# Kernel optimization log

Measured on AMD Instinct MI355X. Metric: run time of the kernel, lower is better.

## Reference

```python
import jax, jax.numpy as jnp
import numpy as np

B, S, D, H = 4, 2048, 1024, 16
HD = D // H


def setup_inputs() -> dict:
    key = jax.random.key(0)
    ks = jax.random.split(key, 9)
    s = 1.0 / np.sqrt(D)
    return {
        "x": jax.random.normal(ks[0], (B, S, D), dtype=jnp.float32),
        "Wq": jax.random.uniform(ks[1], (D, D), jnp.float32, -s, s),
        "bq": jax.random.uniform(ks[2], (D,), jnp.float32, -s, s),
        "Wk": jax.random.uniform(ks[3], (D, D), jnp.float32, -s, s),
        "bk": jax.random.uniform(ks[4], (D,), jnp.float32, -s, s),
        "Wv": jax.random.uniform(ks[5], (D, D), jnp.float32, -s, s),
        "bv": jax.random.uniform(ks[6], (D,), jnp.float32, -s, s),
        "Wo": jax.random.uniform(ks[7], (D, D), jnp.float32, -s, s),
        "bo": jax.random.uniform(ks[8], (D,), jnp.float32, -s, s),
    }


def reference(x, Wq, bq, Wk, bk, Wv, bv, Wo, bo):
    b, s, _ = x.shape
    # projections (torch Linear: y = x @ W.T + b; here W stored as [D,D], use x@W for equivalent math)
    q = (x @ Wq + bq).reshape(b, s, H, HD).transpose(0, 2, 1, 3)  # [b,h,s,hd]
    k = (x @ Wk + bk).reshape(b, s, H, HD).transpose(0, 2, 1, 3)
    v = (x @ Wv + bv).reshape(b, s, H, HD).transpose(0, 2, 1, 3)
    scale = 1.0 / np.sqrt(HD).astype(np.float32)
    scores = jnp.einsum("bhqd,bhkd->bhqk", q, k) * scale  # [b,h,s,s]
    attn = jax.nn.softmax(scores, axis=-1)
    out = jnp.einsum("bhqk,bhkd->bhqd", attn, v)  # [b,h,s,hd]
    out = out.transpose(0, 2, 1, 3).reshape(b, s, D)
    return out @ Wo + bo
```

## Files before the change

### kernel.cpp

```cpp
#include <hip/hip_runtime.h>
#include <hip/hip_bf16.h>

#define NB 4
#define NS 2048
#define ND 1024
#define NH 16
#define NHD 64
#define NM (NB * NS)

typedef __attribute__((ext_vector_type(8))) short bf16x8;
typedef __attribute__((ext_vector_type(4))) float f32x4;
typedef __attribute__((ext_vector_type(16))) float f32x16;
typedef __attribute__((ext_vector_type(4))) unsigned int u32x4;

typedef const unsigned int __attribute__((address_space(1)))* gas_t;
typedef unsigned int __attribute__((address_space(3)))* las_t;

__device__ __forceinline__ void gload_lds16(const void* g, void* l) {
  __builtin_amdgcn_global_load_lds((gas_t)g, (las_t)l, 16, 0, 0);
}

__device__ __forceinline__ unsigned short f2bf(float f) {
  union { __hip_bfloat16 h; unsigned short u; } cv;
  cv.h = __float2bfloat16(f);
  return cv.u;
}

__device__ __forceinline__ unsigned int cvtpk(float a, float b) {
  unsigned int r;
  asm("v_cvt_pk_bf16_f32 %0, %1, %2" : "=v"(r) : "v"(a), "v"(b));
  return r;
}

__device__ __forceinline__ float fexp2(float x) {
  return __builtin_amdgcn_exp2f(x);
}

__global__ __launch_bounds__(256) void convert_x(
    const float* __restrict__ in, uint4* __restrict__ out) {
  const int c = blockIdx.x * 256 + threadIdx.x;
  const float4 a = *(const float4*)(in + (size_t)c * 8);
  const float4 b = *(const float4*)(in + (size_t)c * 8 + 4);
  uint4 u;
  u.x = cvtpk(a.x, a.y); u.y = cvtpk(a.z, a.w);
  u.z = cvtpk(b.x, b.y); u.w = cvtpk(b.z, b.w);
  out[c] = u;
}

__global__ __launch_bounds__(256) void transpose_qkv(
    const float* __restrict__ Wq, const float* __restrict__ Wk,
    const float* __restrict__ Wv, unsigned short* __restrict__ out) {
  __shared__ float tile[64][65];
  const int t = threadIdx.x;
  const int bx = blockIdx.x;
  const int by = blockIdx.y;
  const int which = by >> 4;
  const float* in = which == 0 ? Wq : (which == 1 ? Wk : Wv);
  const int byl = by & 15;
#pragma unroll
  for (int j = 0; j < 4; ++j) {
    const int lin = j * 1024 + t * 4;
    const int r = lin >> 6, c = lin & 63;
    float4 v = *(const float4*)(in + (size_t)(bx * 64 + r) * ND + byl * 64 + c);
    tile[r][c + 0] = v.x; tile[r][c + 1] = v.y;
    tile[r][c + 2] = v.z; tile[r][c + 3] = v.w;
  }
  __syncthreads();
#pragma unroll
  for (int j = 0; j < 4; ++j) {
    const int lin = j * 1024 + t * 4;
    const int r = lin >> 6, c = lin & 63;
    uint2 u;
    u.x = cvtpk(tile[c + 0][r], tile[c + 1][r]);
    u.y = cvtpk(tile[c + 2][r], tile[c + 3][r]);
    *(uint2*)(out + (size_t)(by * 64 + r) * ND + bx * 64 + c) = u;
  }
}

__global__ __launch_bounds__(256) void transpose_w(
    const float* __restrict__ in, unsigned short* __restrict__ out) {
  __shared__ float tile[64][65];
  const int t = threadIdx.x;
  const int bx = blockIdx.x, by = blockIdx.y;
#pragma unroll
  for (int j = 0; j < 4; ++j) {
    const int lin = j * 1024 + t * 4;
    const int r = lin >> 6, c = lin & 63;
    float4 v = *(const float4*)(in + (size_t)(bx * 64 + r) * ND + by * 64 + c);
    tile[r][c + 0] = v.x; tile[r][c + 1] = v.y;
    tile[r][c + 2] = v.z; tile[r][c + 3] = v.w;
  }
  __syncthreads();
#pragma unroll
  for (int j = 0; j < 4; ++j) {
    const int lin = j * 1024 + t * 4;
    const int r = lin >> 6, c = lin & 63;
    uint2 u;
    u.x = cvtpk(tile[c + 0][r], tile[c + 1][r]);
    u.y = cvtpk(tile[c + 2][r], tile[c + 3][r]);
    *(uint2*)(out + (size_t)(by * 64 + r) * ND + bx * 64 + c) = u;
  }
}

__global__ __launch_bounds__(256) void gemm_qkv(
    const unsigned short* __restrict__ Ab, const unsigned short* __restrict__ BT,
    const float* __restrict__ bq, const float* __restrict__ bk,
    const float* __restrict__ bv, unsigned short* __restrict__ Qb,
    unsigned short* __restrict__ Kb, unsigned short* __restrict__ VTb) {
  __shared__ unsigned short As[128 * 64];
  __shared__ unsigned short Bs[128 * 64];
  const int t = threadIdx.x;
  const int w = blockIdx.x;
  const int xcd = w & 7, idx = w >> 3;
  const int mblk = xcd + ((idx / 24) << 3);
  const int nblk = idx % 24;
  const int m0 = mblk * 128, n0 = nblk * 128;
  const int lane = t & 63, wid = t >> 6;
  const int wm = (wid >> 1) * 64, wn = (wid & 1) * 64;
  const int lr = lane & 15, lg = lane >> 4;

  const f32x4 zero4 = {0.f, 0.f, 0.f, 0.f};
  f32x4 acc[4][4];
#pragma unroll
  for (int i = 0; i < 4; ++i)
#pragma unroll
    for (int j = 0; j < 4; ++j) acc[i][j] = zero4;

  for (int k0 = 0; k0 < ND; k0 += 64) {
    __syncthreads();
#pragma unroll
    for (int j = 0; j < 4; ++j) {
      const int id = j * 256 + t;
      const int row = id >> 3, cs8 = id & 7;
      const int cg8 = cs8 ^ (row & 7);
      gload_lds16(BT + (size_t)(n0 + row) * ND + k0 + cg8 * 8, &Bs[id * 8]);
      gload_lds16(Ab + (size_t)(m0 + row) * ND + k0 + cg8 * 8, &As[id * 8]);
    }
    __syncthreads();

#pragma unroll
    for (int kk = 0; kk < 2; ++kk) {
      bf16x8 af[4], bv4[4];
#pragma unroll
      for (int mi = 0; mi < 4; ++mi) {
        const int row = wm + mi * 16 + lr;
        const int slot = (kk * 4 + lg) ^ (row & 7);
        af[mi] = *(const bf16x8*)&As[row * 64 + slot * 8];
      }
#pragma unroll
      for (int ni = 0; ni < 4; ++ni) {
        const int row = wn + ni * 16 + lr;
        const int slot = (kk * 4 + lg) ^ (row & 7);
        bv4[ni] = *(const bf16x8*)&Bs[row * 64 + slot * 8];
      }
      __builtin_amdgcn_s_setprio(1);
#pragma unroll
      for (int mi = 0; mi < 4; ++mi)
#pragma unroll
        for (int ni = 0; ni < 4; ++ni)
          acc[mi][ni] = __builtin_amdgcn_mfma_f32_16x16x32_bf16(
              af[mi], bv4[ni], acc[mi][ni], 0, 0, 0);
      __builtin_amdgcn_s_setprio(0);
    }
  }

#pragma unroll
  for (int mi = 0; mi < 4; ++mi) {
#pragma unroll
    for (int ni = 0; ni < 4; ++ni) {
      const int mbase = m0 + wm + mi * 16 + lg * 4;
      const int n = n0 + wn + ni * 16 + lr;
      const int which = n >> 10, nl = n & 1023;
      const int h = nl >> 6, hd = nl & 63;
      const float bval = which == 0 ? bq[nl] : (which == 1 ? bk[nl] : bv[nl]);
      float vo[4];
#pragma unroll
      for (int i = 0; i < 4; ++i) {
        vo[i] = acc[mi][ni][i] + bval;
        if (which == 0) vo[i] *= 0.18033688f;
      }
      if (which < 2) {
        unsigned short* dst = which == 0 ? Qb : Kb;
#pragma unroll
        for (int i = 0; i < 4; ++i) {
          const int m = mbase + i;
          const int b = m >> 11, s = m & (NS - 1);
          dst[(((size_t)b * NH + h) * NS + s) * NHD + hd] = f2bf(vo[i]);
        }
      } else {
        const int b = mbase >> 11, s = mbase & (NS - 1);
        ushort4 o;
        o.x = f2bf(vo[0]); o.y = f2bf(vo[1]);
        o.z = f2bf(vo[2]); o.w = f2bf(vo[3]);
        *(ushort4*)&VTb[(((size_t)b * NH + h) * NHD + hd) * NS + s] = o;
      }
    }
  }
}

__global__ __launch_bounds__(256) void gemm_out(
    const unsigned short* __restrict__ Ab, const unsigned short* __restrict__ BT,
    const float* __restrict__ bias, float* __restrict__ Cf) {
  __shared__ unsigned short As[128 * 64];
  __shared__ unsigned short Bs[128 * 64];
  const int t = threadIdx.x;
  const int w = blockIdx.x;
  const int mblk = (w & 7) + ((w >> 6) << 3);
  const int nblk = (w >> 3) & 7;
  const int m0 = mblk * 128, n0 = nblk * 128;
  const int lane = t & 63, wid = t >> 6;
  const int wm = (wid >> 1) * 64, wn = (wid & 1) * 64;
  const int lr = lane & 15, lg = lane >> 4;

  const f32x4 zero4 = {0.f, 0.f, 0.f, 0.f};
  f32x4 acc[4][4];
#pragma unroll
  for (int i = 0; i < 4; ++i)
#pragma unroll
    for (int j = 0; j < 4; ++j) acc[i][j] = zero4;

  for (int k0 = 0; k0 < ND; k0 += 64) {
    __syncthreads();
#pragma unroll
    for (int j = 0; j < 4; ++j) {
      const int id = j * 256 + t;
      const int row = id >> 3, cs8 = id & 7;
      const int cg8 = cs8 ^ (row & 7);
      gload_lds16(BT + (size_t)(n0 + row) * ND + k0 + cg8 * 8, &Bs[id * 8]);
      gload_lds16(Ab + (size_t)(m0 + row) * ND + k0 + cg8 * 8, &As[id * 8]);
    }
    __syncthreads();

#pragma unroll
    for (int kk = 0; kk < 2; ++kk) {
      bf16x8 af[4], bv4[4];
#pragma unroll
      for (int mi = 0; mi < 4; ++mi) {
        const int row = wm + mi * 16 + lr;
        const int slot = (kk * 4 + lg) ^ (row & 7);
        af[mi] = *(const bf16x8*)&As[row * 64 + slot * 8];
      }
#pragma unroll
      for (int ni = 0; ni < 4; ++ni) {
        const int row = wn + ni * 16 + lr;
        const int slot = (kk * 4 + lg) ^ (row & 7);
        bv4[ni] = *(const bf16x8*)&Bs[row * 64 + slot * 8];
      }
      __builtin_amdgcn_s_setprio(1);
#pragma unroll
      for (int mi = 0; mi < 4; ++mi)
#pragma unroll
        for (int ni = 0; ni < 4; ++ni)
          acc[mi][ni] = __builtin_amdgcn_mfma_f32_16x16x32_bf16(
              af[mi], bv4[ni], acc[mi][ni], 0, 0, 0);
      __builtin_amdgcn_s_setprio(0);
    }
  }

#pragma unroll
  for (int mi = 0; mi < 4; ++mi) {
#pragma unroll
    for (int ni = 0; ni < 4; ++ni) {
      const int mbase = m0 + wm + mi * 16 + lg * 4;
      const int n = n0 + wn + ni * 16 + lr;
      const float bval = bias[n];
#pragma unroll
      for (int i = 0; i < 4; ++i)
        Cf[(size_t)(mbase + i) * ND + n] = acc[mi][ni][i] + bval;
    }
  }
}

__global__ __launch_bounds__(512) void attn_mfma(
    const unsigned short* __restrict__ Qb, const unsigned short* __restrict__ Kb,
    const unsigned short* __restrict__ VTb, unsigned short* __restrict__ Aout) {
  __shared__ unsigned short S[32768];
  const int t = threadIdx.x, lane = t & 63, wid = t >> 6;
  const int lq = lane & 31, h = lane >> 5;
  const int w = blockIdx.x;
  const int xcd = w & 7, idx = w >> 3;
  const int bh = xcd + ((idx >> 3) << 3);
  const int qtile = idx & 7;
  const size_t hoff = (size_t)bh * NS * NHD;
  const int q0w = qtile * 256 + wid * 32;

  bf16x8 qf[4];
#pragma unroll
  for (int kc = 0; kc < 4; ++kc)
    qf[kc] = *(const bf16x8*)(Qb + hoff + (size_t)(q0w + lq) * NHD + kc * 16 + h * 8);

  const unsigned short* gK[2];
  const unsigned short* gV[2];
  unsigned short* lK[2];
  unsigned short* lV[2];
#pragma unroll
  for (int j = 0; j < 2; ++j) {
    const int c16 = wid * 2 + j;
    gK[j] = Kb + hoff + (size_t)((c16 & 3) * 32 + lq) * NHD + (c16 >> 2) * 16 + h * 8;
    lK[j] = &S[c16 * 512];
    gV[j] = VTb + hoff + (size_t)((c16 & 1) * 32 + lq) * NS + (c16 >> 1) * 16 + h * 8;
    lV[j] = &S[16384 + c16 * 512];
  }

  f32x16 z16 = 0.f;
  f32x16 oacc0 = 0.f, oacc1 = 0.f, lacc = 0.f;
  const short oneb = (short)0x3F80;
  const bf16x8 ones = {oneb, oneb, oneb, oneb, oneb, oneb, oneb, oneb};

  auto stage = [&](int bufofs, int tl) {
    const int kt = (2 * qtile + tl) & 15;
    const size_t kOff = (size_t)kt * (128 * NHD);
    const size_t vOff = (size_t)kt * 128;
#pragma unroll
    for (int j = 0; j < 2; ++j) {
      gload_lds16(gK[j] + kOff, lK[j] + bufofs);
      gload_lds16(gV[j] + vOff, lV[j] + bufofs);
    }
  };

  auto compute = [&](int bufofs) {
    const unsigned short* kb = &S[bufofs] + lane * 8;
    const unsigned short* vb = &S[16384 + bufofs] + lane * 8;
#pragma unroll
    for (int sb = 0; sb < 4; ++sb) {
      __builtin_amdgcn_s_setprio(1);
      f32x16 s;
      {
        bf16x8 k0 = *(const bf16x8*)(kb + sb * 512);
        s = __builtin_amdgcn_mfma_f32_32x32x16_bf16(k0, qf[0], z16, 0, 0, 0);
        bf16x8 k1 = *(const bf16x8*)(kb + sb * 512 + 2048);
        s = __builtin_amdgcn_mfma_f32_32x32x16_bf16(k1, qf[1], s, 0, 0, 0);
        bf16x8 k2 = *(const bf16x8*)(kb + sb * 512 + 4096);
        s = __builtin_amdgcn_mfma_f32_32x32x16_bf16(k2, qf[2], s, 0, 0, 0);
        bf16x8 k3 = *(const bf16x8*)(kb + sb * 512 + 6144);
        s = __builtin_amdgcn_mfma_f32_32x32x16_bf16(k3, qf[3], s, 0, 0, 0);
      }
      __builtin_amdgcn_s_setprio(0);

      unsigned int a0, a1, b0, b1, c0, c1, d0, d1;
      a0 = cvtpk(fexp2(s[0]), fexp2(s[1]));
      a1 = cvtpk(fexp2(s[2]), fexp2(s[3]));
      b0 = cvtpk(fexp2(s[4]), fexp2(s[5]));
      b1 = cvtpk(fexp2(s[6]), fexp2(s[7]));
      c0 = cvtpk(fexp2(s[8]), fexp2(s[9]));
      c1 = cvtpk(fexp2(s[10]), fexp2(s[11]));
      d0 = cvtpk(fexp2(s[12]), fexp2(s[13]));
      d1 = cvtpk(fexp2(s[14]), fexp2(s[15]));
      asm("v_permlane32_swap_b32 %0, %1" : "+v"(a0), "+v"(b0));
      asm("v_permlane32_swap_b32 %0, %1" : "+v"(a1), "+v"(b1));
      asm("v_permlane32_swap_b32 %0, %1" : "+v"(c0), "+v"(d0));
      asm("v_permlane32_swap_b32 %0, %1" : "+v"(c1), "+v"(d1));
      u32x4 plo_u = {a0, a1, b0, b1};
      u32x4 phi_u = {c0, c1, d0, d1};
      const bf16x8 plo = __builtin_bit_cast(bf16x8, plo_u);
      const bf16x8 phi = __builtin_bit_cast(bf16x8, phi_u);

      const int cA = sb * 2048;
      __builtin_amdgcn_s_setprio(1);
      {
        bf16x8 v0 = *(const bf16x8*)(vb + cA);
        oacc0 = __builtin_amdgcn_mfma_f32_32x32x16_bf16(v0, plo, oacc0, 0, 0, 0);
        bf16x8 v1 = *(const bf16x8*)(vb + cA + 512);
        oacc1 = __builtin_amdgcn_mfma_f32_32x32x16_bf16(v1, plo, oacc1, 0, 0, 0);
        lacc = __builtin_amdgcn_mfma_f32_32x32x16_bf16(ones, plo, lacc, 0, 0, 0);
        bf16x8 v2 = *(const bf16x8*)(vb + cA + 1024);
        oacc0 = __builtin_amdgcn_mfma_f32_32x32x16_bf16(v2, phi, oacc0, 0, 0, 0);
        bf16x8 v3 = *(const bf16x8*)(vb + cA + 1536);
        oacc1 = __builtin_amdgcn_mfma_f32_32x32x16_bf16(v3, phi, oacc1, 0, 0, 0);
        lacc = __builtin_amdgcn_mfma_f32_32x32x16_bf16(ones, phi, lacc, 0, 0, 0);
      }
      __builtin_amdgcn_s_setprio(0);
    }
  };

  stage(0, 0);
  __syncthreads();

  for (int i = 0; i < 8; ++i) {
    stage(8192, 2 * i + 1);
    compute(0);
    __syncthreads();
    if (i < 7) stage(0, 2 * i + 2);
    compute(8192);
    __syncthreads();
  }

  const float inv = 1.0f / lacc[0];
  unsigned short* Olds = &S[wid * 2304];
#pragma unroll
  for (int rr = 0; rr < 8; ++rr) {
    const int dl = 2 * (rr & 1) + 8 * (rr >> 1) + 4 * h;
    *(unsigned int*)&Olds[lq * 72 + dl] =
        cvtpk(oacc0[2 * rr] * inv, oacc0[2 * rr + 1] * inv);
    *(unsigned int*)&Olds[lq * 72 + 32 + dl] =
        cvtpk(oacc1[2 * rr] * inv, oacc1[2 * rr + 1] * inv);
  }
  const int b = bh >> 4, hh = bh & 15;
#pragma unroll
  for (int jj = 0; jj < 4; ++jj) {
    const int ci = jj * 64 + lane;
    const int q = ci >> 3, slot = ci & 7;
    const uint4 ov = *(const uint4*)&Olds[q * 72 + slot * 8];
    const int m = b * NS + q0w + q;
    *(uint4*)&Aout[(size_t)m * ND + hh * NHD + slot * 8] = ov;
  }
}

extern "C" void kernel_launch(void* const* d_in, const int* in_sizes, int n_in,
                              void* d_out, int out_size, void* d_ws,
                              size_t ws_size, hipStream_t stream) {
  const float* x  = (const float*)d_in[0];
  const float* Wq = (const float*)d_in[1];
  const float* bq = (const float*)d_in[2];
  const float* Wk = (const float*)d_in[3];
  const float* bk = (const float*)d_in[4];
  const float* Wv = (const float*)d_in[5];
  const float* bv = (const float*)d_in[6];
  const float* Wo = (const float*)d_in[7];
  const float* bo = (const float*)d_in[8];
  float* out = (float*)d_out;

  const size_t BIG = (size_t)NM * ND;
  unsigned short* Qb    = (unsigned short*)d_ws;
  unsigned short* Kb    = Qb + BIG;
  unsigned short* VTb   = Kb + BIG;
  unsigned short* Aattn = VTb + BIG;
  unsigned short* WTqkv = Aattn;
  unsigned short* WTo   = Qb;
  unsigned short* xb    = (unsigned short*)d_out;

  convert_x<<<4096, 256, 0, stream>>>(x, (uint4*)xb);
  transpose_qkv<<<dim3(16, 48), 256, 0, stream>>>(Wq, Wk, Wv, WTqkv);
  gemm_qkv<<<1536, 256, 0, stream>>>(xb, WTqkv, bq, bk, bv, Qb, Kb, VTb);

  attn_mfma<<<512, 512, 0, stream>>>(Qb, Kb, VTb, Aattn);

  transpose_w<<<dim3(16, 16), 256, 0, stream>>>(Wo, WTo);
  gemm_out<<<512, 256, 0, stream>>>(Aattn, WTo, bo, out);
}
```

Baseline: 179.5 us.

## Double-buffer output GEMM LDS tiles and compute softmax denominator with VALU sums

```diff
diff --git a/kernel.cpp b/kernel.cpp
--- a/kernel.cpp
+++ b/kernel.cpp
@@ -10,6 +10,7 @@
 
 typedef __attribute__((ext_vector_type(8))) short bf16x8;
 typedef __attribute__((ext_vector_type(4))) float f32x4;
+typedef __attribute__((ext_vector_type(2))) float f32x2;
 typedef __attribute__((ext_vector_type(16))) float f32x16;
 typedef __attribute__((ext_vector_type(4))) unsigned int u32x4;
 
@@ -201,8 +202,8 @@
 __global__ __launch_bounds__(256) void gemm_out(
     const unsigned short* __restrict__ Ab, const unsigned short* __restrict__ BT,
     const float* __restrict__ bias, float* __restrict__ Cf) {
-  __shared__ unsigned short As[128 * 64];
-  __shared__ unsigned short Bs[128 * 64];
+  __shared__ unsigned short As[2][128 * 64];
+  __shared__ unsigned short Bs[2][128 * 64];
   const int t = threadIdx.x;
   const int w = blockIdx.x;
   const int mblk = (w & 7) + ((w >> 6) << 3);
@@ -219,18 +220,18 @@
 #pragma unroll
     for (int j = 0; j < 4; ++j) acc[i][j] = zero4;
 
-  for (int k0 = 0; k0 < ND; k0 += 64) {
-    __syncthreads();
+  auto stage = [&](int k0, int buf) {
 #pragma unroll
     for (int j = 0; j < 4; ++j) {
       const int id = j * 256 + t;
       const int row = id >> 3, cs8 = id & 7;
       const int cg8 = cs8 ^ (row & 7);
-      gload_lds16(BT + (size_t)(n0 + row) * ND + k0 + cg8 * 8, &Bs[id * 8]);
-      gload_lds16(Ab + (size_t)(m0 + row) * ND + k0 + cg8 * 8, &As[id * 8]);
-    }
-    __syncthreads();
-
+      gload_lds16(BT + (size_t)(n0 + row) * ND + k0 + cg8 * 8, &Bs[buf][id * 8]);
+      gload_lds16(Ab + (size_t)(m0 + row) * ND + k0 + cg8 * 8, &As[buf][id * 8]);
+    }
+  };
+
+  auto compute = [&](int buf) {
 #pragma unroll
     for (int kk = 0; kk < 2; ++kk) {
       bf16x8 af[4], bv4[4];
@@ -238,13 +239,13 @@
       for (int mi = 0; mi < 4; ++mi) {
         const int row = wm + mi * 16 + lr;
         const int slot = (kk * 4 + lg) ^ (row & 7);
-        af[mi] = *(const bf16x8*)&As[row * 64 + slot * 8];
+        af[mi] = *(const bf16x8*)&As[buf][row * 64 + slot * 8];
       }
 #pragma unroll
       for (int ni = 0; ni < 4; ++ni) {
         const int row = wn + ni * 16 + lr;
         const int slot = (kk * 4 + lg) ^ (row & 7);
-        bv4[ni] = *(const bf16x8*)&Bs[row * 64 + slot * 8];
+        bv4[ni] = *(const bf16x8*)&Bs[buf][row * 64 + slot * 8];
       }
       __builtin_amdgcn_s_setprio(1);
 #pragma unroll
@@ -255,6 +256,17 @@
               af[mi], bv4[ni], acc[mi][ni], 0, 0, 0);
       __builtin_amdgcn_s_setprio(0);
     }
+  };
+
+  stage(0, 0);
+  __syncthreads();
+  for (int k0 = 0; k0 < ND; k0 += 128) {
+    stage(k0 + 64, 1);
+    compute(0);
+    __syncthreads();
+    if (k0 + 128 < ND) stage(k0 + 128, 0);
+    compute(1);
+    __syncthreads();
   }
 
 #pragma unroll
@@ -303,9 +315,8 @@
   }
 
   f32x16 z16 = 0.f;
-  f32x16 oacc0 = 0.f, oacc1 = 0.f, lacc = 0.f;
-  const short oneb = (short)0x3F80;
-  const bf16x8 ones = {oneb, oneb, oneb, oneb, oneb, oneb, oneb, oneb};
+  f32x16 oacc0 = 0.f, oacc1 = 0.f;
+  float lsum = 0.f;
 
   auto stage = [&](int bufofs, int tl) {
     const int kt = (2 * qtile + tl) & 15;
@@ -337,15 +348,27 @@
       }
       __builtin_amdgcn_s_setprio(0);
 
+      float ps[16];
+#pragma unroll
+      for (int i = 0; i < 16; ++i) ps[i] = fexp2(s[i]);
+
+      f32x2 acc2 = {0.f, 0.f};
+#pragma unroll
+      for (int i = 0; i < 8; ++i) {
+        f32x2 e = {ps[2 * i], ps[2 * i + 1]};
+        acc2 += e;
+      }
+      lsum += acc2[0] + acc2[1];
+
       unsigned int a0, a1, b0, b1, c0, c1, d0, d1;
-      a0 = cvtpk(fexp2(s[0]), fexp2(s[1]));
-      a1 = cvtpk(fexp2(s[2]), fexp2(s[3]));
-      b0 = cvtpk(fexp2(s[4]), fexp2(s[5]));
-      b1 = cvtpk(fexp2(s[6]), fexp2(s[7]));
-      c0 = cvtpk(fexp2(s[8]), fexp2(s[9]));
-      c1 = cvtpk(fexp2(s[10]), fexp2(s[11]));
-      d0 = cvtpk(fexp2(s[12]), fexp2(s[13]));
-      d1 = cvtpk(fexp2(s[14]), fexp2(s[15]));
+      a0 = cvtpk(ps[0], ps[1]);
+      a1 = cvtpk(ps[2], ps[3]);
+      b0 = cvtpk(ps[4], ps[5]);
+      b1 = cvtpk(ps[6], ps[7]);
+      c0 = cvtpk(ps[8], ps[9]);
+      c1 = cvtpk(ps[10], ps[11]);
+      d0 = cvtpk(ps[12], ps[13]);
+      d1 = cvtpk(ps[14], ps[15]);
       asm("v_permlane32_swap_b32 %0, %1" : "+v"(a0), "+v"(b0));
       asm("v_permlane32_swap_b32 %0, %1" : "+v"(a1), "+v"(b1));
       asm("v_permlane32_swap_b32 %0, %1" : "+v"(c0), "+v"(d0));
@@ -362,12 +385,10 @@
         oacc0 = __builtin_amdgcn_mfma_f32_32x32x16_bf16(v0, plo, oacc0, 0, 0, 0);
         bf16x8 v1 = *(const bf16x8*)(vb + cA + 512);
         oacc1 = __builtin_amdgcn_mfma_f32_32x32x16_bf16(v1, plo, oacc1, 0, 0, 0);
-        lacc = __builtin_amdgcn_mfma_f32_32x32x16_bf16(ones, plo, lacc, 0, 0, 0);
         bf16x8 v2 = *(const bf16x8*)(vb + cA + 1024);
         oacc0 = __builtin_amdgcn_mfma_f32_32x32x16_bf16(v2, phi, oacc0, 0, 0, 0);
         bf16x8 v3 = *(const bf16x8*)(vb + cA + 1536);
         oacc1 = __builtin_amdgcn_mfma_f32_32x32x16_bf16(v3, phi, oacc1, 0, 0, 0);
-        lacc = __builtin_amdgcn_mfma_f32_32x32x16_bf16(ones, phi, lacc, 0, 0, 0);
       }
       __builtin_amdgcn_s_setprio(0);
     }
@@ -385,7 +406,8 @@
     __syncthreads();
   }
 
-  const float inv = 1.0f / lacc[0];
+  const float lsum_tot = lsum + __shfl_xor(lsum, 32);
+  const float inv = 1.0f / lsum_tot;
   unsigned short* Olds = &S[wid * 2304];
 #pragma unroll
   for (int rr = 0; rr < 8; ++rr) {
```

Measured after the change: 190.3 us. 1.06x slower.

## Double-buffer LDS tiles in QKV and output projection GEMMs

Applied to the files above, without the earlier changes.

```diff
diff --git a/kernel.cpp b/kernel.cpp
--- a/kernel.cpp
+++ b/kernel.cpp
@@ -107,8 +107,8 @@
     const float* __restrict__ bq, const float* __restrict__ bk,
     const float* __restrict__ bv, unsigned short* __restrict__ Qb,
     unsigned short* __restrict__ Kb, unsigned short* __restrict__ VTb) {
-  __shared__ unsigned short As[128 * 64];
-  __shared__ unsigned short Bs[128 * 64];
+  __shared__ unsigned short As[2][128 * 64];
+  __shared__ unsigned short Bs[2][128 * 64];
   const int t = threadIdx.x;
   const int w = blockIdx.x;
   const int xcd = w & 7, idx = w >> 3;
@@ -126,18 +126,18 @@
 #pragma unroll
     for (int j = 0; j < 4; ++j) acc[i][j] = zero4;
 
-  for (int k0 = 0; k0 < ND; k0 += 64) {
-    __syncthreads();
+  auto stage = [&](int k0, int buf) {
 #pragma unroll
     for (int j = 0; j < 4; ++j) {
       const int id = j * 256 + t;
       const int row = id >> 3, cs8 = id & 7;
       const int cg8 = cs8 ^ (row & 7);
-      gload_lds16(BT + (size_t)(n0 + row) * ND + k0 + cg8 * 8, &Bs[id * 8]);
-      gload_lds16(Ab + (size_t)(m0 + row) * ND + k0 + cg8 * 8, &As[id * 8]);
-    }
-    __syncthreads();
-
+      gload_lds16(BT + (size_t)(n0 + row) * ND + k0 + cg8 * 8, &Bs[buf][id * 8]);
+      gload_lds16(Ab + (size_t)(m0 + row) * ND + k0 + cg8 * 8, &As[buf][id * 8]);
+    }
+  };
+
+  auto compute = [&](int buf) {
 #pragma unroll
     for (int kk = 0; kk < 2; ++kk) {
       bf16x8 af[4], bv4[4];
@@ -145,13 +145,13 @@
       for (int mi = 0; mi < 4; ++mi) {
         const int row = wm + mi * 16 + lr;
         const int slot = (kk * 4 + lg) ^ (row & 7);
-        af[mi] = *(const bf16x8*)&As[row * 64 + slot * 8];
+        af[mi] = *(const bf16x8*)&As[buf][row * 64 + slot * 8];
       }
 #pragma unroll
       for (int ni = 0; ni < 4; ++ni) {
         const int row = wn + ni * 16 + lr;
         const int slot = (kk * 4 + lg) ^ (row & 7);
-        bv4[ni] = *(const bf16x8*)&Bs[row * 64 + slot * 8];
+        bv4[ni] = *(const bf16x8*)&Bs[buf][row * 64 + slot * 8];
       }
       __builtin_amdgcn_s_setprio(1);
 #pragma unroll
@@ -162,6 +162,17 @@
               af[mi], bv4[ni], acc[mi][ni], 0, 0, 0);
       __builtin_amdgcn_s_setprio(0);
     }
+  };
+
+  stage(0, 0);
+  __syncthreads();
+  for (int k0 = 0; k0 < ND; k0 += 128) {
+    stage(k0 + 64, 1);
+    compute(0);
+    __syncthreads();
+    if (k0 + 128 < ND) stage(k0 + 128, 0);
+    compute(1);
+    __syncthreads();
   }
 
 #pragma unroll
@@ -201,8 +212,8 @@
 __global__ __launch_bounds__(256) void gemm_out(
     const unsigned short* __restrict__ Ab, const unsigned short* __restrict__ BT,
     const float* __restrict__ bias, float* __restrict__ Cf) {
-  __shared__ unsigned short As[128 * 64];
-  __shared__ unsigned short Bs[128 * 64];
+  __shared__ unsigned short As[2][128 * 64];
+  __shared__ unsigned short Bs[2][128 * 64];
   const int t = threadIdx.x;
   const int w = blockIdx.x;
   const int mblk = (w & 7) + ((w >> 6) << 3);
@@ -219,18 +230,18 @@
 #pragma unroll
     for (int j = 0; j < 4; ++j) acc[i][j] = zero4;
 
-  for (int k0 = 0; k0 < ND; k0 += 64) {
-    __syncthreads();
+  auto stage = [&](int k0, int buf) {
 #pragma unroll
     for (int j = 0; j < 4; ++j) {
       const int id = j * 256 + t;
       const int row = id >> 3, cs8 = id & 7;
       const int cg8 = cs8 ^ (row & 7);
-      gload_lds16(BT + (size_t)(n0 + row) * ND + k0 + cg8 * 8, &Bs[id * 8]);
-      gload_lds16(Ab + (size_t)(m0 + row) * ND + k0 + cg8 * 8, &As[id * 8]);
-    }
-    __syncthreads();
-
+      gload_lds16(BT + (size_t)(n0 + row) * ND + k0 + cg8 * 8, &Bs[buf][id * 8]);
+      gload_lds16(Ab + (size_t)(m0 + row) * ND + k0 + cg8 * 8, &As[buf][id * 8]);
+    }
+  };
+
+  auto compute = [&](int buf) {
 #pragma unroll
     for (int kk = 0; kk < 2; ++kk) {
       bf16x8 af[4], bv4[4];
@@ -238,13 +249,13 @@
       for (int mi = 0; mi < 4; ++mi) {
         const int row = wm + mi * 16 + lr;
         const int slot = (kk * 4 + lg) ^ (row & 7);
-        af[mi] = *(const bf16x8*)&As[row * 64 + slot * 8];
+        af[mi] = *(const bf16x8*)&As[buf][row * 64 + slot * 8];
       }
 #pragma unroll
       for (int ni = 0; ni < 4; ++ni) {
         const int row = wn + ni * 16 + lr;
         const int slot = (kk * 4 + lg) ^ (row & 7);
-        bv4[ni] = *(const bf16x8*)&Bs[row * 64 + slot * 8];
+        bv4[ni] = *(const bf16x8*)&Bs[buf][row * 64 + slot * 8];
       }
       __builtin_amdgcn_s_setprio(1);
 #pragma unroll
@@ -255,6 +266,17 @@
               af[mi], bv4[ni], acc[mi][ni], 0, 0, 0);
       __builtin_amdgcn_s_setprio(0);
     }
+  };
+
+  stage(0, 0);
+  __syncthreads();
+  for (int k0 = 0; k0 < ND; k0 += 128) {
+    stage(k0 + 64, 1);
+    compute(0);
+    __syncthreads();
+    if (k0 + 128 < ND) stage(k0 + 128, 0);
+    compute(1);
+    __syncthreads();
   }
 
 #pragma unroll
```

Result: no change. 180.4 us (+0.5%).
